# Optimization experiments

Measured on AMD Instinct MI355X. Metric: run time of the kernel, lower is better.

The kernel has to match this reference:

```python
import jax, jax.numpy as jnp
import numpy as np

B, N, DIM, M_DIM, FOURIER = 2, 512, 64, 16, 4
EDGE_IN = FOURIER * 2 + DIM * 2 + 1  # 137


def _mk_params(key):
    ks = jax.random.split(key, 12)
    s = 0.02
    p = {}
    p['w1e'] = jax.random.normal(ks[0], (EDGE_IN, EDGE_IN * 2), jnp.float32) * s
    p['b1e'] = jnp.zeros((EDGE_IN * 2,), jnp.float32)
    p['w2e'] = jax.random.normal(ks[1], (EDGE_IN * 2, M_DIM), jnp.float32) * s
    p['b2e'] = jnp.zeros((M_DIM,), jnp.float32)
    p['w1c'] = jax.random.normal(ks[2], (M_DIM, M_DIM * 4), jnp.float32) * s
    p['b1c'] = jnp.zeros((M_DIM * 4,), jnp.float32)
    p['w2c'] = jax.random.normal(ks[3], (M_DIM * 4, 1), jnp.float32) * s
    p['b2c'] = jnp.zeros((1,), jnp.float32)
    p['w1h'] = jax.random.normal(ks[4], (DIM + M_DIM, DIM * 2), jnp.float32) * s
    p['b1h'] = jnp.zeros((DIM * 2,), jnp.float32)
    p['w2h'] = jax.random.normal(ks[5], (DIM * 2, DIM), jnp.float32) * s
    p['b2h'] = jnp.zeros((DIM,), jnp.float32)
    return p


def setup_inputs() -> dict:
    key = jax.random.key(0)
    kf, kc, kp = jax.random.split(key, 3)
    inp = {
        'feats': jax.random.normal(kf, (B, N, DIM), jnp.float32),
        'coors': jax.random.normal(kc, (B, N, 3), jnp.float32),
    }
    inp.update(_mk_params(kp))
    return inp


def _fourier_encode_dist(x, num_encodings):
    # x: [b, i, j, 1]
    orig = x[..., None]  # [b,i,j,1,1]
    scales = 2.0 ** jnp.arange(num_encodings, dtype=x.dtype)
    xs = orig / scales  # [b,i,j,1,E]
    enc = jnp.concatenate([jnp.sin(xs), jnp.cos(xs), orig], axis=-1)  # [b,i,j,1,2E+1]
    return enc[..., 0, :]  # [b,i,j,2E+1]


def _safe_norm(rel_coors):
    sq = jnp.sum(rel_coors * rel_coors, axis=-1, keepdims=True)
    # grad-safe sqrt: torch.norm has 0 subgradient at 0
    return jnp.where(sq > 0, jnp.sqrt(jnp.where(sq > 0, sq, 1.0)), 0.0)


def _egnn_forward(feats, coors, w1e, b1e, w2e, b2e, w1c, b1c, w2c, b2c, w1h, b1h, w2h, b2h):
    b, n, d = feats.shape
    rel_coors = coors[:, :, None, :] - coors[:, None, :, :]  # [b,i,j,3]
    rel_dist = _safe_norm(rel_coors)  # [b,i,j,1]
    rel_dist = _fourier_encode_dist(rel_dist, FOURIER)  # [b,i,j,2F+1]
    feats_i = jnp.broadcast_to(feats[:, :, None, :], (b, n, n, d))
    feats_j = jnp.broadcast_to(feats[:, None, :, :], (b, n, n, d))
    edge_input = jnp.concatenate([feats_i, feats_j, rel_dist], axis=-1)  # [b,i,j,EDGE_IN]
    h = jax.nn.relu(edge_input @ w1e + b1e)
    m_ij = h @ w2e + b2e  # [b,i,j,m]
    cw = jax.nn.relu(m_ij @ w1c + b1c) @ w2c + b2c  # [b,i,j,1]
    coor_weights = cw[..., 0]  # [b,i,j]
    coors_out = jnp.einsum('bij,bijc->bic', coor_weights, rel_coors)
    m_i = jnp.sum(m_ij, axis=-2)  # [b,i,m]
    hid_in = jnp.concatenate([feats, m_i], axis=-1)
    hidden_out = jax.nn.relu(hid_in @ w1h + b1h) @ w2h + b2h
    return hidden_out, coors_out


def reference(feats, coors, w1e, b1e, w2e, b2e, w1c, b1c, w2c, b2c, w1h, b1h, w2h, b2h):
    return _egnn_forward(feats, coors, w1e, b1e, w2e, b2e, w1c, b1c, w2c, b2c, w1h, b1h, w2h, b2h)
```

## Files before the change

### kernel.cpp

```cpp
#include <hip/hip_runtime.h>
#include <math.h>
#include <stdint.h>

#define NP 288
#define OUT_H (2*512*64)

typedef _Float16 f16;
typedef __attribute__((ext_vector_type(2))) _Float16 f16x2;
typedef __attribute__((ext_vector_type(4))) _Float16 f16x4;
typedef __attribute__((ext_vector_type(8))) _Float16 f16x8;
typedef __attribute__((ext_vector_type(4))) float f32x4;

static __device__ __forceinline__ f16x2 pkrtz(float a, float b) {
    return __builtin_bit_cast(f16x2, __builtin_amdgcn_cvt_pkrtz(a, b));
}

#if defined(__has_builtin)
#if __has_builtin(__builtin_amdgcn_mfma_f32_16x16x16f16)
#define HAVE_MFMA16 1
#endif
#endif

static __device__ __forceinline__ f32x4 mfma16(f16x4 a, f16x4 b, f32x4 c) {
#ifdef HAVE_MFMA16
    return __builtin_amdgcn_mfma_f32_16x16x16f16(a, b, c, 0, 0, 0);
#else
    f32x4 d;
    asm volatile("v_mfma_f32_16x16x16_f16 %0, %1, %2, %3\n\ts_nop 7\n\ts_nop 7"
                 : "=v"(d) : "v"(a), "v"(b), "v"(c));
    return d;
#endif
}

static __device__ __forceinline__ f16x4 relupack(f32x4 h) {
    f16x2 lo = pkrtz(h[0], h[1]);
    f16x2 hi = pkrtz(h[2], h[3]);
    const f16x2 z = {(_Float16)0, (_Float16)0};
    lo = __builtin_elementwise_max(lo, z);
    hi = __builtin_elementwise_max(hi, z);
    return __builtin_shufflevector(lo, hi, 0, 1, 2, 3);
}

__global__ __launch_bounds__(256) void egnn_pre(
    const float* __restrict__ feats, const float* __restrict__ w1e,
    const float* __restrict__ b1e,   const float* __restrict__ w2e,
    const float* __restrict__ w1c,
    f16* __restrict__ Q1, f16* __restrict__ P2F, f16* __restrict__ Wd,
    f16* __restrict__ W2F, f16* __restrict__ W1CB)
{
    int id = blockIdx.x * 256 + threadIdx.x;
    const int NN = 1024 * NP;
    if (id < 2 * NN) {
        int hf = id / NN, r = id % NN;
        int n = r / NP, e = r % NP;
        float a = 0.f;
        if (e < 274) {
            a = hf ? 0.f : b1e[e];
            const float* fp = feats + n * 64;
            const float* wp = w1e + hf * 64 * 274 + e;
            #pragma unroll 8
            for (int d2 = 0; d2 < 64; ++d2) a += fp[d2] * wp[d2 * 274];
        }
        if (hf) {
            int b = n >> 9, j = n & 511;
            int jt = j >> 4, cl = j & 15;
            int S = e >> 4, gg = (e >> 2) & 3, jj = e & 3;
            P2F[(((b * 32 + jt) * 18 + S) * 64 + (cl + 16 * gg)) * 4 + jj] = (f16)a;
        } else {
            Q1[n * NP + e] = (f16)a;
        }
    } else {
        int x = id - 2 * NN;
        if (x < 9 * NP) {
            int e = x % NP, k = x / NP;
            Wd[x] = (f16)(e < 274 ? w1e[(128 + k) * 274 + e] : 0.f);
        } else if (x < 9 * NP + 1152) {
            int y = x - 9 * NP;
            int S = y >> 6, l = y & 63, cc = l & 15, gg = l >> 4;
            f16x4 v = {0, 0, 0, 0};
            #pragma unroll
            for (int jj = 0; jj < 4; ++jj) {
                int e = S * 16 + gg * 4 + jj;
                v[jj] = (f16)(e < 274 ? w2e[e * 16 + cc] : 0.f);
            }
            *(f16x4*)(W2F + y * 4) = v;
        } else if (x < 9 * NP + 1152 + 2048) {
            int y = x - 9 * NP - 1152;
            int T = y >> 9, rem = y & 511, c2 = rem >> 5, k = rem & 31;
            W1CB[y] = (f16)(k < 16 ? w1c[k * 64 + T * 16 + c2] : 0.f);
        }
    }
}

__global__ __launch_bounds__(256) void egnn_edge(
    const float* __restrict__ feats, const float* __restrict__ coors,
    const float* __restrict__ b2e,   const float* __restrict__ b1c,
    const float* __restrict__ w2c,   const float* __restrict__ b2cv,
    const float* __restrict__ w1h,   const float* __restrict__ b1h,
    const float* __restrict__ w2h,   const float* __restrict__ b2h,
    const f16* __restrict__ Q1,  const f16* __restrict__ P2F,
    const f16* __restrict__ Wd,  const f16* __restrict__ W2F,
    const f16* __restrict__ W1CB, float* __restrict__ out)
{
    __shared__ f16x4 sA1f[1152];
    __shared__ f16x4 sB2f[1152];
    __shared__ __align__(16) f16 sM[512 * 16];
    __shared__ float sHid[128];
    __shared__ float sRedM[4][16];
    __shared__ float sRedC[4][3];
    __shared__ float sFin[16];

    const int bi = blockIdx.x, bb = bi >> 9;
    const int t = threadIdx.x;
    const int lane = t & 63, wv = t >> 6;
    const int c = lane & 15, g = lane >> 4;

    {
        const uint2* src = (const uint2*)W2F;
        uint2* dst = (uint2*)sB2f;
        for (int x = t; x < 1152; x += 256) dst[x] = src[x];
        const f16* Q1r = Q1 + bi * NP;
        for (int x = t; x < 1152; x += 256) {
            int S = x >> 6, l = x & 63, cc = l & 15, gg = l >> 4;
            int e = S * 16 + cc;
            f16x4 v = {0, 0, 0, 0};
            if (gg == 0)      { v[0]=Wd[0*NP+e]; v[1]=Wd[1*NP+e]; v[2]=Wd[2*NP+e]; v[3]=Wd[3*NP+e]; }
            else if (gg == 1) { v[0]=Wd[4*NP+e]; v[1]=Wd[5*NP+e]; v[2]=Wd[6*NP+e]; v[3]=Wd[7*NP+e]; }
            else if (gg == 2) { v[0]=Wd[8*NP+e]; v[1]=Q1r[e]; }
            sA1f[x] = v;
        }
    }
    const float b2e_c = b2e[c];
    const float cix = coors[bi * 3 + 0];
    const float ciy = coors[bi * 3 + 1];
    const float ciz = coors[bi * 3 + 2];
    __syncthreads();

    const f16* P2Fb = P2F + (bb << 5) * 18 * 256;

    #pragma unroll 1
    for (int pass = 0; pass < 2; ++pass) {
        const int jbase = wv * 128 + pass * 64;
        #pragma unroll 1
        for (int pr = 0; pr < 2; ++pr) {
            f16x4 b1u[2];
            const f16* cpp[2];
            #pragma unroll
            for (int u = 0; u < 2; ++u) {
                const int jt = (jbase >> 4) + pr * 2 + u;
                const int j = jbase + (pr * 2 + u) * 16 + c;
                const int jg = (bb << 9) + j;
                float rx = cix - coors[jg * 3 + 0];
                float ry = ciy - coors[jg * 3 + 1];
                float rz = ciz - coors[jg * 3 + 2];
                float sq = rx * rx + ry * ry + rz * rz;
                float d = sq > 0.f ? sqrtf(sq) : 0.f;
                float en[8];
                #pragma unroll
                for (int k = 0; k < 4; ++k)
                    __sincosf(d * (1.f / (float)(1 << k)), &en[k], &en[4 + k]);
                f16x2 p01 = pkrtz(en[0], en[1]);
                f16x2 p23 = pkrtz(en[2], en[3]);
                f16x2 p45 = pkrtz(en[4], en[5]);
                f16x2 p67 = pkrtz(en[6], en[7]);
                f16x2 pd1 = pkrtz(d, 1.0f);
                f16x2 zz = {(_Float16)0, (_Float16)0};
                f16x2 lo = (g == 0) ? p01 : (g == 1) ? p45 : (g == 2) ? pd1 : zz;
                f16x2 hi = (g == 0) ? p23 : (g == 1) ? p67 : zz;
                b1u[u] = __builtin_shufflevector(lo, hi, 0, 1, 2, 3);
                cpp[u] = P2Fb + jt * 18 * 256 + lane * 4;
            }

            f32x4 acc0 = {0,0,0,0}, acc1 = {0,0,0,0};
            f16x4 c0A = *(const f16x4*)(cpp[0]);
            f16x4 c0B = *(const f16x4*)(cpp[1]);
            f16x4 c1A = *(const f16x4*)(cpp[0] + 256);
            f16x4 c1B = *(const f16x4*)(cpp[1] + 256);
            f16x4 n0A = *(const f16x4*)(cpp[0] + 512);
            f16x4 n0B = *(const f16x4*)(cpp[1] + 512);
            f16x4 n1A = *(const f16x4*)(cpp[0] + 768);
            f16x4 n1B = *(const f16x4*)(cpp[1] + 768);

            #pragma unroll
            for (int S2 = 0; S2 < 9; ++S2) {
                const int S = 2 * S2;
                f16x4 m0A = c0A, m0B = c0B, m1A = c1A, m1B = c1B;
                if (S2 < 7) {
                    m0A = *(const f16x4*)(cpp[0] + (S + 4) * 256);
                    m0B = *(const f16x4*)(cpp[1] + (S + 4) * 256);
                    m1A = *(const f16x4*)(cpp[0] + (S + 5) * 256);
                    m1B = *(const f16x4*)(cpp[1] + (S + 5) * 256);
                }
                {
                    f16x4 a1 = sA1f[S * 64 + lane];
                    f16x4 b2 = sB2f[S * 64 + lane];
                    f32x4 cf0 = {(float)c0A[0], (float)c0A[1], (float)c0A[2], (float)c0A[3]};
                    f32x4 cf1 = {(float)c0B[0], (float)c0B[1], (float)c0B[2], (float)c0B[3]};
                    f32x4 h0 = mfma16(a1, b1u[0], cf0);
                    f32x4 h1 = mfma16(a1, b1u[1], cf1);
                    acc0 = mfma16(relupack(h0), b2, acc0);
                    acc1 = mfma16(relupack(h1), b2, acc1);
                }
                {
                    f16x4 a1 = sA1f[(S + 1) * 64 + lane];
                    f16x4 b2 = sB2f[(S + 1) * 64 + lane];
                    f32x4 cf0 = {(float)c1A[0], (float)c1A[1], (float)c1A[2], (float)c1A[3]};
                    f32x4 cf1 = {(float)c1B[0], (float)c1B[1], (float)c1B[2], (float)c1B[3]};
                    f32x4 h0 = mfma16(a1, b1u[0], cf0);
                    f32x4 h1 = mfma16(a1, b1u[1], cf1);
                    acc0 = mfma16(relupack(h0), b2, acc0);
                    acc1 = mfma16(relupack(h1), b2, acc1);
                }
                c0A = n0A; c0B = n0B; c1A = n1A; c1B = n1B;
                n0A = m0A; n0B = m0B; n1A = m1A; n1B = m1B;
            }

            #pragma unroll
            for (int u = 0; u < 2; ++u) {
                const int jr = jbase + (pr * 2 + u) * 16 + g * 4;
                const f32x4 accu = u ? acc1 : acc0;
                #pragma unroll
                for (int r = 0; r < 4; ++r)
                    sM[(jr + r) * 16 + c] = (f16)(accu[r] + b2e_c);
            }
        }
    }
    __syncthreads();

    f16x8 aW[4];
    f32x4 b1cL[4], w2cL[4];
    #pragma unroll
    for (int T = 0; T < 4; ++T) {
        aW[T] = *(const f16x8*)(W1CB + (T * 16 + c) * 32 + g * 8);
        b1cL[T] = *(const f32x4*)(b1c + T * 16 + g * 4);
        w2cL[T] = *(const f32x4*)(w2c + T * 16 + g * 4);
    }
    const float b2c0 = b2cv[0];

    float cax = 0.f, cay = 0.f, caz = 0.f;
    float macc8[8] = {0.f,0.f,0.f,0.f,0.f,0.f,0.f,0.f};

    #pragma unroll 1
    for (int jt = 0; jt < 8; ++jt) {
        const int jrow = wv * 128 + jt * 16;
        f16x8 bm = {0,0,0,0,0,0,0,0};
        if (g < 2) {
            bm = *(const f16x8*)(sM + (jrow + c) * 16 + g * 8);
            #pragma unroll
            for (int p = 0; p < 8; ++p) macc8[p] += (float)bm[p];
        }
        f32x4 zc = {0,0,0,0};
        float cwp = 0.f;
        #pragma unroll
        for (int T = 0; T < 4; ++T) {
            f32x4 hd = __builtin_amdgcn_mfma_f32_16x16x32_f16(aW[T], bm, zc, 0, 0, 0);
            #pragma unroll
            for (int r = 0; r < 4; ++r)
                cwp += fmaxf(hd[r] + b1cL[T][r], 0.f) * w2cL[T][r];
        }
        cwp += __shfl_xor(cwp, 16);
        cwp += __shfl_xor(cwp, 32);
        float cw = cwp + b2c0;

        int jg = (bb << 9) + jrow + c;
        float rx = cix - coors[jg * 3 + 0];
        float ry = ciy - coors[jg * 3 + 1];
        float rz = ciz - coors[jg * 3 + 2];
        cax += cw * rx; cay += cw * ry; caz += cw * rz;
    }

    #pragma unroll
    for (int msk = 1; msk <= 8; msk <<= 1)
        #pragma unroll
        for (int p = 0; p < 8; ++p) macc8[p] += __shfl_xor(macc8[p], msk);
    if (c == 0 && g < 2) {
        #pragma unroll
        for (int p = 0; p < 8; ++p) sRedM[wv][g * 8 + p] = macc8[p];
    }
    #pragma unroll
    for (int msk = 1; msk <= 32; msk <<= 1) {
        cax += __shfl_xor(cax, msk);
        cay += __shfl_xor(cay, msk);
        caz += __shfl_xor(caz, msk);
    }
    if (lane == 0) { sRedC[wv][0] = cax; sRedC[wv][1] = cay; sRedC[wv][2] = caz; }
    __syncthreads();

    if (t < 16) sFin[t] = sRedM[0][t] + sRedM[1][t] + sRedM[2][t] + sRedM[3][t];
    if (t >= 32 && t < 35) {
        int k = t - 32;
        out[OUT_H + bi * 3 + k] =
            (sRedC[0][k] + sRedC[1][k] + sRedC[2][k] + sRedC[3][k]) * 0.25f;
    }
    __syncthreads();

    if (t < 128) {
        float a = b1h[t];
        const float* fp = feats + bi * 64;
        #pragma unroll 8
        for (int k = 0; k < 64; ++k) a += fp[k] * w1h[k * 128 + t];
        #pragma unroll
        for (int k = 0; k < 16; ++k) a += sFin[k] * w1h[(64 + k) * 128 + t];
        sHid[t] = fmaxf(a, 0.f);
    }
    __syncthreads();
    if (t < 64) {
        float a = b2h[t];
        #pragma unroll 8
        for (int k = 0; k < 128; ++k) a += sHid[k] * w2h[k * 64 + t];
        out[bi * 64 + t] = a;
    }
}

extern "C" void kernel_launch(void* const* d_in, const int* in_sizes, int n_in,
                              void* d_out, int out_size, void* d_ws, size_t ws_size,
                              hipStream_t stream)
{
    const float* feats = (const float*)d_in[0];
    const float* coors = (const float*)d_in[1];
    const float* w1e   = (const float*)d_in[2];
    const float* b1e   = (const float*)d_in[3];
    const float* w2e   = (const float*)d_in[4];
    const float* b2e   = (const float*)d_in[5];
    const float* w1c   = (const float*)d_in[6];
    const float* b1c   = (const float*)d_in[7];
    const float* w2c   = (const float*)d_in[8];
    const float* b2c   = (const float*)d_in[9];
    const float* w1h   = (const float*)d_in[10];
    const float* b1h   = (const float*)d_in[11];
    const float* w2h   = (const float*)d_in[12];
    const float* b2h   = (const float*)d_in[13];
    float* out = (float*)d_out;

    char* ws = (char*)d_ws;
    f16* Q1   = (f16*)ws;
    f16* P2F  = (f16*)(ws + 589824);
    f16* Wd   = (f16*)(ws + 1179648);
    f16* W2F  = (f16*)(ws + 1179648 + 5184);
    f16* W1CB = (f16*)(ws + 1179648 + 5184 + 9216);

    egnn_pre<<<2327, 256, 0, stream>>>(feats, w1e, b1e, w2e, w1c, Q1, P2F, Wd, W2F, W1CB);
    egnn_edge<<<1024, 256, 0, stream>>>(feats, coors, b2e, b1c, w2c, b2c,
                                        w1h, b1h, w2h, b2h,
                                        Q1, P2F, Wd, W2F, W1CB, out);
}
```

Measured before the change: 65.49 us.

## Store P2F projection in fp32 and derive Fourier sincos by double-angle

The precomputed feats_j projection P2F is now stored in fp32 instead of fp16. The edge kernel loads it straight into the MFMA accumulator, which removes the per-element fp16-to-fp32 conversions. The prefetch depth drops from two stages to one. The four sincos evaluations are replaced by one sincos at the smallest scale plus double-angle recurrences, cutting transcendental work. The trade-off is twice the global traffic and workspace for P2F, less latency hiding, and some accuracy drift from the recurrence.

```diff
diff --git a/kernel.cpp b/kernel.cpp
--- a/kernel.cpp
+++ b/kernel.cpp
@@ -45,7 +45,7 @@
     const float* __restrict__ feats, const float* __restrict__ w1e,
     const float* __restrict__ b1e,   const float* __restrict__ w2e,
     const float* __restrict__ w1c,
-    f16* __restrict__ Q1, f16* __restrict__ P2F, f16* __restrict__ Wd,
+    f16* __restrict__ Q1, float* __restrict__ P2F, f16* __restrict__ Wd,
     f16* __restrict__ W2F, f16* __restrict__ W1CB)
 {
     int id = blockIdx.x * 256 + threadIdx.x;
@@ -65,7 +65,7 @@
             int b = n >> 9, j = n & 511;
             int jt = j >> 4, cl = j & 15;
             int S = e >> 4, gg = (e >> 2) & 3, jj = e & 3;
-            P2F[(((b * 32 + jt) * 18 + S) * 64 + (cl + 16 * gg)) * 4 + jj] = (f16)a;
+            P2F[(((b * 32 + jt) * 18 + S) * 64 + (cl + 16 * gg)) * 4 + jj] = a;
         } else {
             Q1[n * NP + e] = (f16)a;
         }
@@ -98,7 +98,7 @@
     const float* __restrict__ w2c,   const float* __restrict__ b2cv,
     const float* __restrict__ w1h,   const float* __restrict__ b1h,
     const float* __restrict__ w2h,   const float* __restrict__ b2h,
-    const f16* __restrict__ Q1,  const f16* __restrict__ P2F,
+    const f16* __restrict__ Q1,  const float* __restrict__ P2F,
     const f16* __restrict__ Wd,  const f16* __restrict__ W2F,
     const f16* __restrict__ W1CB, float* __restrict__ out)
 {
@@ -136,7 +136,7 @@
     const float ciz = coors[bi * 3 + 2];
     __syncthreads();
 
-    const f16* P2Fb = P2F + (bb << 5) * 18 * 256;
+    const float* P2Fb = P2F + (bb << 5) * 18 * 256;
 
     #pragma unroll 1
     for (int pass = 0; pass < 2; ++pass) {
@@ -144,7 +144,7 @@
         #pragma unroll 1
         for (int pr = 0; pr < 2; ++pr) {
             f16x4 b1u[2];
-            const f16* cpp[2];
+            const float* cpp[2];
             #pragma unroll
             for (int u = 0; u < 2; ++u) {
                 const int jt = (jbase >> 4) + pr * 2 + u;
@@ -155,14 +155,15 @@
                 float rz = ciz - coors[jg * 3 + 2];
                 float sq = rx * rx + ry * ry + rz * rz;
                 float d = sq > 0.f ? sqrtf(sq) : 0.f;
-                float en[8];
-                #pragma unroll
-                for (int k = 0; k < 4; ++k)
-                    __sincosf(d * (1.f / (float)(1 << k)), &en[k], &en[4 + k]);
-                f16x2 p01 = pkrtz(en[0], en[1]);
-                f16x2 p23 = pkrtz(en[2], en[3]);
-                f16x2 p45 = pkrtz(en[4], en[5]);
-                f16x2 p67 = pkrtz(en[6], en[7]);
+                float s8, c8v;
+                __sincosf(d * 0.125f, &s8, &c8v);
+                float s4 = 2.f * s8 * c8v, c4v = 1.f - 2.f * s8 * s8;
+                float s2 = 2.f * s4 * c4v, c2v = 1.f - 2.f * s4 * s4;
+                float s1 = 2.f * s2 * c2v, c1v = 1.f - 2.f * s2 * s2;
+                f16x2 p01 = pkrtz(s1, s2);
+                f16x2 p23 = pkrtz(s4, s8);
+                f16x2 p45 = pkrtz(c1v, c2v);
+                f16x2 p67 = pkrtz(c4v, c8v);
                 f16x2 pd1 = pkrtz(d, 1.0f);
                 f16x2 zz = {(_Float16)0, (_Float16)0};
                 f16x2 lo = (g == 0) ? p01 : (g == 1) ? p45 : (g == 2) ? pd1 : zz;
@@ -172,47 +173,38 @@
             }
 
             f32x4 acc0 = {0,0,0,0}, acc1 = {0,0,0,0};
-            f16x4 c0A = *(const f16x4*)(cpp[0]);
-            f16x4 c0B = *(const f16x4*)(cpp[1]);
-            f16x4 c1A = *(const f16x4*)(cpp[0] + 256);
-            f16x4 c1B = *(const f16x4*)(cpp[1] + 256);
-            f16x4 n0A = *(const f16x4*)(cpp[0] + 512);
-            f16x4 n0B = *(const f16x4*)(cpp[1] + 512);
-            f16x4 n1A = *(const f16x4*)(cpp[0] + 768);
-            f16x4 n1B = *(const f16x4*)(cpp[1] + 768);
+            f32x4 c0A = *(const f32x4*)(cpp[0]);
+            f32x4 c0B = *(const f32x4*)(cpp[1]);
+            f32x4 c1A = *(const f32x4*)(cpp[0] + 256);
+            f32x4 c1B = *(const f32x4*)(cpp[1] + 256);
 
             #pragma unroll
             for (int S2 = 0; S2 < 9; ++S2) {
                 const int S = 2 * S2;
-                f16x4 m0A = c0A, m0B = c0B, m1A = c1A, m1B = c1B;
-                if (S2 < 7) {
-                    m0A = *(const f16x4*)(cpp[0] + (S + 4) * 256);
-                    m0B = *(const f16x4*)(cpp[1] + (S + 4) * 256);
-                    m1A = *(const f16x4*)(cpp[0] + (S + 5) * 256);
-                    m1B = *(const f16x4*)(cpp[1] + (S + 5) * 256);
+                f32x4 n0A, n0B, n1A, n1B;
+                if (S2 < 8) {
+                    n0A = *(const f32x4*)(cpp[0] + (S + 2) * 256);
+                    n0B = *(const f32x4*)(cpp[1] + (S + 2) * 256);
+                    n1A = *(const f32x4*)(cpp[0] + (S + 3) * 256);
+                    n1B = *(const f32x4*)(cpp[1] + (S + 3) * 256);
                 }
                 {
                     f16x4 a1 = sA1f[S * 64 + lane];
                     f16x4 b2 = sB2f[S * 64 + lane];
-                    f32x4 cf0 = {(float)c0A[0], (float)c0A[1], (float)c0A[2], (float)c0A[3]};
-                    f32x4 cf1 = {(float)c0B[0], (float)c0B[1], (float)c0B[2], (float)c0B[3]};
-                    f32x4 h0 = mfma16(a1, b1u[0], cf0);
-                    f32x4 h1 = mfma16(a1, b1u[1], cf1);
+                    f32x4 h0 = mfma16(a1, b1u[0], c0A);
+                    f32x4 h1 = mfma16(a1, b1u[1], c0B);
                     acc0 = mfma16(relupack(h0), b2, acc0);
                     acc1 = mfma16(relupack(h1), b2, acc1);
                 }
                 {
                     f16x4 a1 = sA1f[(S + 1) * 64 + lane];
                     f16x4 b2 = sB2f[(S + 1) * 64 + lane];
-                    f32x4 cf0 = {(float)c1A[0], (float)c1A[1], (float)c1A[2], (float)c1A[3]};
-                    f32x4 cf1 = {(float)c1B[0], (float)c1B[1], (float)c1B[2], (float)c1B[3]};
-                    f32x4 h0 = mfma16(a1, b1u[0], cf0);
-                    f32x4 h1 = mfma16(a1, b1u[1], cf1);
+                    f32x4 h0 = mfma16(a1, b1u[0], c1A);
+                    f32x4 h1 = mfma16(a1, b1u[1], c1B);
                     acc0 = mfma16(relupack(h0), b2, acc0);
                     acc1 = mfma16(relupack(h1), b2, acc1);
                 }
                 c0A = n0A; c0B = n0B; c1A = n1A; c1B = n1B;
-                n0A = m0A; n0B = m0B; n1A = m1A; n1B = m1B;
             }
 
             #pragma unroll
@@ -333,11 +325,11 @@
     float* out = (float*)d_out;
 
     char* ws = (char*)d_ws;
-    f16* Q1   = (f16*)ws;
-    f16* P2F  = (f16*)(ws + 589824);
-    f16* Wd   = (f16*)(ws + 1179648);
-    f16* W2F  = (f16*)(ws + 1179648 + 5184);
-    f16* W1CB = (f16*)(ws + 1179648 + 5184 + 9216);
+    f16*   Q1   = (f16*)ws;
+    float* P2F  = (float*)(ws + 589824);
+    f16*   Wd   = (f16*)(ws + 589824 + 1179648);
+    f16*   W2F  = (f16*)(ws + 589824 + 1179648 + 5184);
+    f16*   W1CB = (f16*)(ws + 589824 + 1179648 + 5184 + 9216);
 
     egnn_pre<<<2327, 256, 0, stream>>>(feats, w1e, b1e, w2e, w1c, Q1, P2F, Wd, W2F, W1CB);
     egnn_edge<<<1024, 256, 0, stream>>>(feats, coors, b2e, b1c, w2c, b2c,
```

Result: no change. 64.57 us (-1.4%).

## Split edge kernel over j halves with partial sums and separate node-update kernel

Applied to the files above, without the earlier changes.

The edge kernel now runs two blocks per node i, each covering half of the j range. Partial message and coordinate sums go to workspace, and a new small kernel combines them and runs the node MLP. The goal is more blocks and higher occupancy through halved LDS and launch bounds of 8, with a shallower prefetch pipeline to save registers. Fourier features now come from one sincos call plus double-angle recurrences instead of four sincos calls. The cost is an extra kernel launch, a global round trip for the partials, and the staging of shared weights done twice per i.

```diff
diff --git a/kernel.cpp b/kernel.cpp
--- a/kernel.cpp
+++ b/kernel.cpp
@@ -92,25 +92,24 @@
     }
 }
 
-__global__ __launch_bounds__(256) void egnn_edge(
-    const float* __restrict__ feats, const float* __restrict__ coors,
+__global__ __launch_bounds__(256, 8) void egnn_edge(
+    const float* __restrict__ coors,
     const float* __restrict__ b2e,   const float* __restrict__ b1c,
     const float* __restrict__ w2c,   const float* __restrict__ b2cv,
-    const float* __restrict__ w1h,   const float* __restrict__ b1h,
-    const float* __restrict__ w2h,   const float* __restrict__ b2h,
     const f16* __restrict__ Q1,  const f16* __restrict__ P2F,
     const f16* __restrict__ Wd,  const f16* __restrict__ W2F,
-    const f16* __restrict__ W1CB, float* __restrict__ out)
+    const f16* __restrict__ W1CB,
+    float* __restrict__ partM, float* __restrict__ partC)
 {
     __shared__ f16x4 sA1f[1152];
     __shared__ f16x4 sB2f[1152];
-    __shared__ __align__(16) f16 sM[512 * 16];
-    __shared__ float sHid[128];
+    __shared__ __align__(16) f16 sM[256 * 16];
     __shared__ float sRedM[4][16];
     __shared__ float sRedC[4][3];
-    __shared__ float sFin[16];
-
-    const int bi = blockIdx.x, bb = bi >> 9;
+
+    const int blk = blockIdx.x;
+    const int bi = blk >> 1, half = blk & 1;
+    const int bb = bi >> 9;
     const int t = threadIdx.x;
     const int lane = t & 63, wv = t >> 6;
     const int c = lane & 15, g = lane >> 4;
@@ -138,91 +137,85 @@
 
     const f16* P2Fb = P2F + (bb << 5) * 18 * 256;
 
+    const int jl0 = wv * 64;
     #pragma unroll 1
-    for (int pass = 0; pass < 2; ++pass) {
-        const int jbase = wv * 128 + pass * 64;
-        #pragma unroll 1
-        for (int pr = 0; pr < 2; ++pr) {
-            f16x4 b1u[2];
-            const f16* cpp[2];
+    for (int pr = 0; pr < 2; ++pr) {
+        f16x4 b1u[2];
+        const f16* cpp[2];
+        #pragma unroll
+        for (int u = 0; u < 2; ++u) {
+            const int up = pr * 2 + u;
+            const int jt = (half << 4) + (wv << 2) + up;
+            const int j  = (half << 8) + jl0 + up * 16 + c;
+            const int jg = (bb << 9) + j;
+            float rx = cix - coors[jg * 3 + 0];
+            float ry = ciy - coors[jg * 3 + 1];
+            float rz = ciz - coors[jg * 3 + 2];
+            float sq = rx * rx + ry * ry + rz * rz;
+            float d = sq > 0.f ? sqrtf(sq) : 0.f;
+            float s8, c8v;
+            __sincosf(d * 0.125f, &s8, &c8v);
+            float s4 = 2.f * s8 * c8v, c4v = 1.f - 2.f * s8 * s8;
+            float s2 = 2.f * s4 * c4v, c2v = 1.f - 2.f * s4 * s4;
+            float s1 = 2.f * s2 * c2v, c1v = 1.f - 2.f * s2 * s2;
+            f16x2 p01 = pkrtz(s1, s2);
+            f16x2 p23 = pkrtz(s4, s8);
+            f16x2 p45 = pkrtz(c1v, c2v);
+            f16x2 p67 = pkrtz(c4v, c8v);
+            f16x2 pd1 = pkrtz(d, 1.0f);
+            f16x2 zz = {(_Float16)0, (_Float16)0};
+            f16x2 lo = (g == 0) ? p01 : (g == 1) ? p45 : (g == 2) ? pd1 : zz;
+            f16x2 hi = (g == 0) ? p23 : (g == 1) ? p67 : zz;
+            b1u[u] = __builtin_shufflevector(lo, hi, 0, 1, 2, 3);
+            cpp[u] = P2Fb + jt * 18 * 256 + lane * 4;
+        }
+
+        f32x4 acc0 = {0,0,0,0}, acc1 = {0,0,0,0};
+        f16x4 c0A = *(const f16x4*)(cpp[0]);
+        f16x4 c0B = *(const f16x4*)(cpp[1]);
+        f16x4 c1A = *(const f16x4*)(cpp[0] + 256);
+        f16x4 c1B = *(const f16x4*)(cpp[1] + 256);
+
+        #pragma unroll
+        for (int S2 = 0; S2 < 9; ++S2) {
+            const int S = 2 * S2;
+            f16x4 n0A, n0B, n1A, n1B;
+            if (S2 < 8) {
+                n0A = *(const f16x4*)(cpp[0] + (S + 2) * 256);
+                n0B = *(const f16x4*)(cpp[1] + (S + 2) * 256);
+                n1A = *(const f16x4*)(cpp[0] + (S + 3) * 256);
+                n1B = *(const f16x4*)(cpp[1] + (S + 3) * 256);
+            }
+            {
+                f16x4 a1 = sA1f[S * 64 + lane];
+                f16x4 b2 = sB2f[S * 64 + lane];
+                f32x4 cf0 = {(float)c0A[0], (float)c0A[1], (float)c0A[2], (float)c0A[3]};
+                f32x4 cf1 = {(float)c0B[0], (float)c0B[1], (float)c0B[2], (float)c0B[3]};
+                f32x4 h0 = mfma16(a1, b1u[0], cf0);
+                f32x4 h1 = mfma16(a1, b1u[1], cf1);
+                acc0 = mfma16(relupack(h0), b2, acc0);
+                acc1 = mfma16(relupack(h1), b2, acc1);
+            }
+            {
+                f16x4 a1 = sA1f[(S + 1) * 64 + lane];
+                f16x4 b2 = sB2f[(S + 1) * 64 + lane];
+                f32x4 cf0 = {(float)c1A[0], (float)c1A[1], (float)c1A[2], (float)c1A[3]};
+                f32x4 cf1 = {(float)c1B[0], (float)c1B[1], (float)c1B[2], (float)c1B[3]};
+                f32x4 h0 = mfma16(a1, b1u[0], cf0);
+                f32x4 h1 = mfma16(a1, b1u[1], cf1);
+                acc0 = mfma16(relupack(h0), b2, acc0);
+                acc1 = mfma16(relupack(h1), b2, acc1);
+            }
+            c0A = n0A; c0B = n0B; c1A = n1A; c1B = n1B;
+        }
+
+        #pragma unroll
+        for (int u = 0; u < 2; ++u) {
+            const int jr = jl0 + (pr * 2 + u) * 16 + g * 4;
+            const f32x4 accu = u ? acc1 : acc0;
             #pragma unroll
-            for (int u = 0; u < 2; ++u) {
-                const int jt = (jbase >> 4) + pr * 2 + u;
-                const int j = jbase + (pr * 2 + u) * 16 + c;
-                const int jg = (bb << 9) + j;
-                float rx = cix - coors[jg * 3 + 0];
-                float ry = ciy - coors[jg * 3 + 1];
-                float rz = ciz - coors[jg * 3 + 2];
-                float sq = rx * rx + ry * ry + rz * rz;
-                float d = sq > 0.f ? sqrtf(sq) : 0.f;
-                float en[8];
-                #pragma unroll
-                for (int k = 0; k < 4; ++k)
-                    __sincosf(d * (1.f / (float)(1 << k)), &en[k], &en[4 + k]);
-                f16x2 p01 = pkrtz(en[0], en[1]);
-                f16x2 p23 = pkrtz(en[2], en[3]);
-                f16x2 p45 = pkrtz(en[4], en[5]);
-                f16x2 p67 = pkrtz(en[6], en[7]);
-                f16x2 pd1 = pkrtz(d, 1.0f);
-                f16x2 zz = {(_Float16)0, (_Float16)0};
-                f16x2 lo = (g == 0) ? p01 : (g == 1) ? p45 : (g == 2) ? pd1 : zz;
-                f16x2 hi = (g == 0) ? p23 : (g == 1) ? p67 : zz;
-                b1u[u] = __builtin_shufflevector(lo, hi, 0, 1, 2, 3);
-                cpp[u] = P2Fb + jt * 18 * 256 + lane * 4;
-            }
-
-            f32x4 acc0 = {0,0,0,0}, acc1 = {0,0,0,0};
-            f16x4 c0A = *(const f16x4*)(cpp[0]);
-            f16x4 c0B = *(const f16x4*)(cpp[1]);
-            f16x4 c1A = *(const f16x4*)(cpp[0] + 256);
-            f16x4 c1B = *(const f16x4*)(cpp[1] + 256);
-            f16x4 n0A = *(const f16x4*)(cpp[0] + 512);
-            f16x4 n0B = *(const f16x4*)(cpp[1] + 512);
-            f16x4 n1A = *(const f16x4*)(cpp[0] + 768);
-            f16x4 n1B = *(const f16x4*)(cpp[1] + 768);
-
-            #pragma unroll
-            for (int S2 = 0; S2 < 9; ++S2) {
-                const int S = 2 * S2;
-                f16x4 m0A = c0A, m0B = c0B, m1A = c1A, m1B = c1B;
-                if (S2 < 7) {
-                    m0A = *(const f16x4*)(cpp[0] + (S + 4) * 256);
-                    m0B = *(const f16x4*)(cpp[1] + (S + 4) * 256);
-                    m1A = *(const f16x4*)(cpp[0] + (S + 5) * 256);
-                    m1B = *(const f16x4*)(cpp[1] + (S + 5) * 256);
-                }
-                {
-                    f16x4 a1 = sA1f[S * 64 + lane];
-                    f16x4 b2 = sB2f[S * 64 + lane];
-                    f32x4 cf0 = {(float)c0A[0], (float)c0A[1], (float)c0A[2], (float)c0A[3]};
-                    f32x4 cf1 = {(float)c0B[0], (float)c0B[1], (float)c0B[2], (float)c0B[3]};
-                    f32x4 h0 = mfma16(a1, b1u[0], cf0);
-                    f32x4 h1 = mfma16(a1, b1u[1], cf1);
-                    acc0 = mfma16(relupack(h0), b2, acc0);
-                    acc1 = mfma16(relupack(h1), b2, acc1);
-                }
-                {
-                    f16x4 a1 = sA1f[(S + 1) * 64 + lane];
-                    f16x4 b2 = sB2f[(S + 1) * 64 + lane];
-                    f32x4 cf0 = {(float)c1A[0], (float)c1A[1], (float)c1A[2], (float)c1A[3]};
-                    f32x4 cf1 = {(float)c1B[0], (float)c1B[1], (float)c1B[2], (float)c1B[3]};
-                    f32x4 h0 = mfma16(a1, b1u[0], cf0);
-                    f32x4 h1 = mfma16(a1, b1u[1], cf1);
-                    acc0 = mfma16(relupack(h0), b2, acc0);
-                    acc1 = mfma16(relupack(h1), b2, acc1);
-                }
-                c0A = n0A; c0B = n0B; c1A = n1A; c1B = n1B;
-                n0A = m0A; n0B = m0B; n1A = m1A; n1B = m1B;
-            }
-
-            #pragma unroll
-            for (int u = 0; u < 2; ++u) {
-                const int jr = jbase + (pr * 2 + u) * 16 + g * 4;
-                const f32x4 accu = u ? acc1 : acc0;
-                #pragma unroll
-                for (int r = 0; r < 4; ++r)
-                    sM[(jr + r) * 16 + c] = (f16)(accu[r] + b2e_c);
-            }
+            for (int r = 0; r < 4; ++r)
+                sM[(jr + r) * 16 + c] = (f16)(accu[r] + b2e_c);
         }
     }
     __syncthreads();
@@ -241,8 +234,8 @@
     float macc8[8] = {0.f,0.f,0.f,0.f,0.f,0.f,0.f,0.f};
 
     #pragma unroll 1
-    for (int jt = 0; jt < 8; ++jt) {
-        const int jrow = wv * 128 + jt * 16;
+    for (int jt2 = 0; jt2 < 4; ++jt2) {
+        const int jrow = jl0 + jt2 * 16;
         f16x8 bm = {0,0,0,0,0,0,0,0};
         if (g < 2) {
             bm = *(const f16x8*)(sM + (jrow + c) * 16 + g * 8);
@@ -262,7 +255,7 @@
         cwp += __shfl_xor(cwp, 32);
         float cw = cwp + b2c0;
 
-        int jg = (bb << 9) + jrow + c;
+        int jg = (bb << 9) + (half << 8) + jrow + c;
         float rx = cix - coors[jg * 3 + 0];
         float ry = ciy - coors[jg * 3 + 1];
         float rz = ciz - coors[jg * 3 + 2];
@@ -286,29 +279,48 @@
     if (lane == 0) { sRedC[wv][0] = cax; sRedC[wv][1] = cay; sRedC[wv][2] = caz; }
     __syncthreads();
 
-    if (t < 16) sFin[t] = sRedM[0][t] + sRedM[1][t] + sRedM[2][t] + sRedM[3][t];
+    if (t < 16)
+        partM[blk * 16 + t] = sRedM[0][t] + sRedM[1][t] + sRedM[2][t] + sRedM[3][t];
+    if (t >= 32 && t < 35) {
+        int k = t - 32;
+        partC[blk * 3 + k] = sRedC[0][k] + sRedC[1][k] + sRedC[2][k] + sRedC[3][k];
+    }
+}
+
+__global__ __launch_bounds__(128) void egnn_fin(
+    const float* __restrict__ feats,
+    const float* __restrict__ w1h, const float* __restrict__ b1h,
+    const float* __restrict__ w2h, const float* __restrict__ b2h,
+    const float* __restrict__ partM, const float* __restrict__ partC,
+    float* __restrict__ out)
+{
+    const int bi = blockIdx.x;
+    const int t = threadIdx.x;
+    __shared__ float sFin[16];
+    __shared__ float sHid[128];
+
+    if (t < 16) sFin[t] = partM[(2 * bi) * 16 + t] + partM[(2 * bi + 1) * 16 + t];
     if (t >= 32 && t < 35) {
         int k = t - 32;
         out[OUT_H + bi * 3 + k] =
-            (sRedC[0][k] + sRedC[1][k] + sRedC[2][k] + sRedC[3][k]) * 0.25f;
-    }
-    __syncthreads();
-
-    if (t < 128) {
-        float a = b1h[t];
-        const float* fp = feats + bi * 64;
+            (partC[(2 * bi) * 3 + k] + partC[(2 * bi + 1) * 3 + k]) * 0.25f;
+    }
+    __syncthreads();
+
+    float a = b1h[t];
+    const float* fp = feats + bi * 64;
+    #pragma unroll 8
+    for (int k = 0; k < 64; ++k) a += fp[k] * w1h[k * 128 + t];
+    #pragma unroll
+    for (int k = 0; k < 16; ++k) a += sFin[k] * w1h[(64 + k) * 128 + t];
+    sHid[t] = fmaxf(a, 0.f);
+    __syncthreads();
+
+    if (t < 64) {
+        float b = b2h[t];
         #pragma unroll 8
-        for (int k = 0; k < 64; ++k) a += fp[k] * w1h[k * 128 + t];
-        #pragma unroll
-        for (int k = 0; k < 16; ++k) a += sFin[k] * w1h[(64 + k) * 128 + t];
-        sHid[t] = fmaxf(a, 0.f);
-    }
-    __syncthreads();
-    if (t < 64) {
-        float a = b2h[t];
-        #pragma unroll 8
-        for (int k = 0; k < 128; ++k) a += sHid[k] * w2h[k * 64 + t];
-        out[bi * 64 + t] = a;
+        for (int k = 0; k < 128; ++k) b += sHid[k] * w2h[k * 64 + t];
+        out[bi * 64 + t] = b;
     }
 }
 
@@ -333,14 +345,16 @@
     float* out = (float*)d_out;
 
     char* ws = (char*)d_ws;
-    f16* Q1   = (f16*)ws;
-    f16* P2F  = (f16*)(ws + 589824);
-    f16* Wd   = (f16*)(ws + 1179648);
-    f16* W2F  = (f16*)(ws + 1179648 + 5184);
-    f16* W1CB = (f16*)(ws + 1179648 + 5184 + 9216);
+    f16*   Q1    = (f16*)ws;
+    f16*   P2F   = (f16*)(ws + 589824);
+    f16*   Wd    = (f16*)(ws + 1179648);
+    f16*   W2F   = (f16*)(ws + 1184832);
+    f16*   W1CB  = (f16*)(ws + 1194048);
+    float* partM = (float*)(ws + 1198144);
+    float* partC = (float*)(ws + 1329216);
 
     egnn_pre<<<2327, 256, 0, stream>>>(feats, w1e, b1e, w2e, w1c, Q1, P2F, Wd, W2F, W1CB);
-    egnn_edge<<<1024, 256, 0, stream>>>(feats, coors, b2e, b1c, w2c, b2c,
-                                        w1h, b1h, w2h, b2h,
-                                        Q1, P2F, Wd, W2F, W1CB, out);
-}
+    egnn_edge<<<2048, 256, 0, stream>>>(coors, b2e, b1c, w2c, b2c,
+                                        Q1, P2F, Wd, W2F, W1CB, partM, partC);
+    egnn_fin<<<1024, 128, 0, stream>>>(feats, w1h, b1h, w2h, b2h, partM, partC, out);
+}
```

New measurement: 68.63 us. 1.05x slower.
